# Performance work log

Hardware: AMD Instinct MI355X
Metric: run time of the kernel (lower is better)

Reference implementation:

```python
import jax, jax.numpy as jnp
import numpy as np

D_MODEL = 1024
BATCH = 4
SEQ = 4096

def setup_inputs() -> dict:
    key = jax.random.key(0)
    k1, k2, k3, k4 = jax.random.split(key, 4)
    scale = 1.0 / np.sqrt(D_MODEL)
    return {
        "inp_emb": jax.random.normal(k1, (BATCH, SEQ, D_MODEL), dtype=jnp.float32),
        "Wq": jax.random.normal(k2, (D_MODEL, D_MODEL), dtype=jnp.float32) * scale,
        "Wk": jax.random.normal(k3, (D_MODEL, D_MODEL), dtype=jnp.float32) * scale,
        "Wv": jax.random.normal(k4, (D_MODEL, D_MODEL), dtype=jnp.float32) * scale,
    }

def reference(inp_emb, Wq, Wk, Wv):
    d_model = Wq.shape[0]
    # torch Linear (no bias): y = x @ W.T
    Q = jnp.einsum('bsd,ed->bse', inp_emb, Wq)
    K = jnp.einsum('bsd,ed->bse', inp_emb, Wk)
    V = jnp.einsum('bsd,ed->bse', inp_emb, Wv)
    scores = jnp.einsum('bqd,bkd->bqk', Q, K) / jnp.sqrt(jnp.float32(d_model))
    probs = jax.nn.softmax(scores, axis=2)
    return jnp.einsum('bqk,bkd->bqd', probs, V)
```

## Files before the change

kernel.cpp:

```cpp
#include <hip/hip_runtime.h>


typedef __bf16 bf16_t;
typedef __bf16 bf16x8 __attribute__((ext_vector_type(8)));
typedef float f32x4 __attribute__((ext_vector_type(4)));

typedef __attribute__((address_space(3))) void lds_void_t;
typedef __attribute__((address_space(1))) void gbl_void_t;

#define SEQ 4096
#define DM  1024

__global__ __launch_bounds__(256) void cast_f32_to_bf16(
    const float* __restrict__ in, bf16_t* __restrict__ out, int n8)
{
    int idx = blockIdx.x * 256 + threadIdx.x;
    if (idx >= n8) return;
    long i = (long)idx * 8;
    f32x4 a = *(const f32x4*)(in + i);
    f32x4 b = *(const f32x4*)(in + i + 4);
    bf16x8 o;
    o[0] = (bf16_t)a[0]; o[1] = (bf16_t)a[1]; o[2] = (bf16_t)a[2]; o[3] = (bf16_t)a[3];
    o[4] = (bf16_t)b[0]; o[5] = (bf16_t)b[1]; o[6] = (bf16_t)b[2]; o[7] = (bf16_t)b[3];
    *(bf16x8*)(out + i) = o;
}

__global__ __launch_bounds__(256) void cast3_w(
    const float* __restrict__ w0, const float* __restrict__ w1,
    const float* __restrict__ w2, bf16_t* __restrict__ out)
{
    const float* in = (blockIdx.z == 0) ? w0 : (blockIdx.z == 1) ? w1 : w2;
    long i = ((long)blockIdx.x * 256 + threadIdx.x) * 8;
    f32x4 a = *(const f32x4*)(in + i);
    f32x4 b = *(const f32x4*)(in + i + 4);
    bf16x8 o;
    o[0] = (bf16_t)a[0]; o[1] = (bf16_t)a[1]; o[2] = (bf16_t)a[2]; o[3] = (bf16_t)a[3];
    o[4] = (bf16_t)b[0]; o[5] = (bf16_t)b[1]; o[6] = (bf16_t)b[2]; o[7] = (bf16_t)b[3];
    *(bf16x8*)(out + (long)blockIdx.z * 1048576 + i) = o;
}

__global__ __launch_bounds__(256) void zero_f32(float* __restrict__ p, int n)
{
    int idx = blockIdx.x * 256 + threadIdx.x;
    if (idx < n) p[idx] = 0.f;
}

template <typename TOUT, int MODE>
__global__ __launch_bounds__(256, 4) void gemm_bt(
    const bf16_t* __restrict__ A, int lda, long sAz,
    const bf16_t* __restrict__ B, int ldb, long sBz,
    TOUT* __restrict__ C, int ldc, long sCz,
    int K, float scale, float* __restrict__ l, long sLz)
{
    __shared__ bf16_t As[128 * 32];
    __shared__ bf16_t Bs[128 * 32];

    A += (long)blockIdx.z * sAz;
    B += (long)blockIdx.z * sBz;
    C += (long)blockIdx.z * sCz;

    const int tid  = threadIdx.x;
    const int wave = tid >> 6;
    const int lane = tid & 63;
    const int m0 = blockIdx.x * 128;
    const int n0 = blockIdx.y * 128;
    const int wm = (wave >> 1) * 64;
    const int wn = (wave & 1) * 64;
    const int mrow = lane & 15;
    const int koff = (lane >> 4) * 8;

    f32x4 acc[4][4];
#pragma unroll
    for (int i = 0; i < 4; ++i)
#pragma unroll
        for (int j = 0; j < 4; ++j)
            acc[i][j] = (f32x4){0.f, 0.f, 0.f, 0.f};

    const int c0 = wave * 2;

    for (int k0 = 0; k0 < K; k0 += 32) {
#pragma unroll
        for (int t = 0; t < 2; ++t) {
            const int chunk = c0 + t;
            const int flat  = chunk * 64 + lane;
            const int row   = flat >> 2;
            const int kp    = (flat & 3) * 8;
            const bf16_t* ga = A + (long)(m0 + row) * lda + (k0 + kp);
            const bf16_t* gb = B + (long)(n0 + row) * ldb + (k0 + kp);
            __builtin_amdgcn_global_load_lds((const gbl_void_t*)ga,
                                             (lds_void_t*)(As + chunk * 512), 16, 0, 0);
            __builtin_amdgcn_global_load_lds((const gbl_void_t*)gb,
                                             (lds_void_t*)(Bs + chunk * 512), 16, 0, 0);
        }
        __syncthreads();

        bf16x8 af[4], bfr[4];
#pragma unroll
        for (int i = 0; i < 4; ++i)
            af[i] = *(const bf16x8*)(As + (wm + i * 16 + mrow) * 32 + koff);
#pragma unroll
        for (int j = 0; j < 4; ++j)
            bfr[j] = *(const bf16x8*)(Bs + (wn + j * 16 + mrow) * 32 + koff);
#pragma unroll
        for (int i = 0; i < 4; ++i)
#pragma unroll
            for (int j = 0; j < 4; ++j)
                acc[i][j] = __builtin_amdgcn_mfma_f32_16x16x32_bf16(af[i], bfr[j], acc[i][j], 0, 0, 0);
        __syncthreads();
    }

    const int col = lane & 15;
    const int r0  = (lane >> 4) * 4;

    if (MODE == 1) {
#pragma unroll
        for (int i = 0; i < 4; ++i)
#pragma unroll
            for (int r = 0; r < 4; ++r) {
                float s = 0.f;
#pragma unroll
                for (int j = 0; j < 4; ++j) {
                    float e = __expf(acc[i][j][r] * scale);
                    acc[i][j][r] = e;
                    s += e;
                }
                s += __shfl_xor(s, 1);
                s += __shfl_xor(s, 2);
                s += __shfl_xor(s, 4);
                s += __shfl_xor(s, 8);
                if (col == 0)
                    atomicAdd(&l[(long)blockIdx.z * sLz + m0 + wm + i * 16 + r0 + r], s);
            }
#pragma unroll
        for (int i = 0; i < 4; ++i)
#pragma unroll
            for (int j = 0; j < 4; ++j)
#pragma unroll
                for (int r = 0; r < 4; ++r)
                    C[(long)(m0 + wm + i * 16 + r0 + r) * ldc + (n0 + wn + j * 16 + col)] =
                        (TOUT)acc[i][j][r];
    } else if (MODE == 2) {
        float inv[4][4];
#pragma unroll
        for (int i = 0; i < 4; ++i)
#pragma unroll
            for (int r = 0; r < 4; ++r)
                inv[i][r] = scale / l[(long)blockIdx.z * sLz + m0 + wm + i * 16 + r0 + r];
#pragma unroll
        for (int i = 0; i < 4; ++i)
#pragma unroll
            for (int j = 0; j < 4; ++j)
#pragma unroll
                for (int r = 0; r < 4; ++r)
                    C[(long)(m0 + wm + i * 16 + r0 + r) * ldc + (n0 + wn + j * 16 + col)] =
                        (TOUT)(acc[i][j][r] * inv[i][r]);
    } else {
#pragma unroll
        for (int i = 0; i < 4; ++i)
#pragma unroll
            for (int j = 0; j < 4; ++j)
#pragma unroll
                for (int r = 0; r < 4; ++r)
                    C[(long)(m0 + wm + i * 16 + r0 + r) * ldc + (n0 + wn + j * 16 + col)] =
                        (TOUT)(acc[i][j][r] * scale);
    }
}

template <typename TOUT, int MODE>
__global__ __launch_bounds__(512, 2) void gemm_bt256(
    const bf16_t* __restrict__ A, int lda, long sAz,
    const bf16_t* __restrict__ B, int ldb, long sBz,
    TOUT* __restrict__ C, int ldc, long sCz,
    int K, float scale, float* __restrict__ l, long sLz)
{
    __shared__ __align__(1024) char smem[98304];

    A += (long)blockIdx.z * sAz;
    B += (long)blockIdx.z * sBz;
    C += (long)blockIdx.z * sCz;

    const int tid  = threadIdx.x;
    const int wave = tid >> 6;
    const int lane = tid & 63;
    const int m0 = blockIdx.x * 256;
    const int n0 = blockIdx.y * 256;
    const int wm = (wave >> 2) * 128;
    const int wn = (wave & 3) * 64;

    const int srow = wave * 16 + (lane >> 2);
    const int skk  = ((lane & 3) * 8) ^ ((lane & 32) ? 16 : 0);
    const bf16_t* gA0 = A + (long)(m0 + srow) * lda + skk;
    const bf16_t* gA1 = A + (long)(m0 + srow + 128) * lda + skk;
    const bf16_t* gB0 = B + (long)(n0 + srow) * ldb + skk;
    const bf16_t* gB1 = B + (long)(n0 + srow + 128) * ldb + skk;
    char* ldsA = smem + wave * 1024;
    char* ldsB = smem + 49152 + wave * 1024;

    auto stage_A = [&](int kt, int d) {
        const int k0 = kt << 5;
        __builtin_amdgcn_global_load_lds((const gbl_void_t*)(gA0 + k0),
                                         (lds_void_t*)(ldsA + d * 16384), 16, 0, 0);
        __builtin_amdgcn_global_load_lds((const gbl_void_t*)(gA1 + k0),
                                         (lds_void_t*)(ldsA + d * 16384 + 8192), 16, 0, 0);
    };
    auto stage_B = [&](int kt, int d) {
        const int k0 = kt << 5;
        __builtin_amdgcn_global_load_lds((const gbl_void_t*)(gB0 + k0),
                                         (lds_void_t*)(ldsB + d * 16384), 16, 0, 0);
        __builtin_amdgcn_global_load_lds((const gbl_void_t*)(gB1 + k0),
                                         (lds_void_t*)(ldsB + d * 16384 + 8192), 16, 0, 0);
    };

    const int kswz = ((lane >> 4) * 16) ^ ((lane & 8) ? 32 : 0);
    const int aoff = (wm + (lane & 15)) * 64 + kswz;
    const int boff = (wn + (lane & 15)) * 64 + kswz;

    f32x4 acc[8][4];
#pragma unroll
    for (int i = 0; i < 8; ++i)
#pragma unroll
        for (int j = 0; j < 4; ++j)
            acc[i][j] = (f32x4){0.f, 0.f, 0.f, 0.f};

    const int NT = K >> 5;

    stage_A(0, 0); stage_B(0, 0);
    if (NT > 1) {
        stage_A(1, 1); stage_B(1, 1);
        asm volatile("s_waitcnt vmcnt(4)" ::: "memory");
    } else {
        asm volatile("s_waitcnt vmcnt(0)" ::: "memory");
    }
    __builtin_amdgcn_s_barrier();

    int cur = 0, nxt = 2;
    for (int t = 0; t < NT; ++t) {
        const char* pa = smem + cur * 16384 + aoff;
        const char* pb = smem + 49152 + cur * 16384 + boff;

        bf16x8 bfr[4], af[4];
#pragma unroll
        for (int j = 0; j < 4; ++j) bfr[j] = *(const bf16x8*)(pb + j * 1024);
#pragma unroll
        for (int i = 0; i < 4; ++i) af[i] = *(const bf16x8*)(pa + i * 1024);
        if (t + 2 < NT) stage_A(t + 2, nxt);
        __builtin_amdgcn_s_setprio(1);
#pragma unroll
        for (int i = 0; i < 4; ++i)
#pragma unroll
            for (int j = 0; j < 4; ++j)
                acc[i][j] = __builtin_amdgcn_mfma_f32_16x16x32_bf16(af[i], bfr[j], acc[i][j], 0, 0, 0);
        __builtin_amdgcn_s_setprio(0);

        bf16x8 af2[4];
#pragma unroll
        for (int i = 0; i < 4; ++i) af2[i] = *(const bf16x8*)(pa + 4096 + i * 1024);
        if (t + 2 < NT) stage_B(t + 2, nxt);
        __builtin_amdgcn_s_setprio(1);
#pragma unroll
        for (int i = 0; i < 4; ++i)
#pragma unroll
            for (int j = 0; j < 4; ++j)
                acc[4 + i][j] = __builtin_amdgcn_mfma_f32_16x16x32_bf16(af2[i], bfr[j], acc[4 + i][j], 0, 0, 0);
        __builtin_amdgcn_s_setprio(0);

        __builtin_amdgcn_sched_barrier(0);
        if (t + 2 < NT)
            asm volatile("s_waitcnt vmcnt(4) lgkmcnt(0)" ::: "memory");
        else if (t + 1 < NT)
            asm volatile("s_waitcnt vmcnt(0) lgkmcnt(0)" ::: "memory");
        else
            asm volatile("s_waitcnt lgkmcnt(0)" ::: "memory");
        __builtin_amdgcn_s_barrier();
        cur = (cur == 2) ? 0 : cur + 1;
        nxt = (nxt == 2) ? 0 : nxt + 1;
    }

    const int col = lane & 15;
    const int r0  = (lane >> 4) * 4;

    if (MODE == 1) {
#pragma unroll
        for (int i = 0; i < 8; ++i)
#pragma unroll
            for (int r = 0; r < 4; ++r) {
                float s = 0.f;
#pragma unroll
                for (int j = 0; j < 4; ++j) {
                    float e = __expf(acc[i][j][r] * scale);
                    acc[i][j][r] = e;
                    s += e;
                }
                s += __shfl_xor(s, 1);
                s += __shfl_xor(s, 2);
                s += __shfl_xor(s, 4);
                s += __shfl_xor(s, 8);
                if (col == 0)
                    atomicAdd(&l[(long)blockIdx.z * sLz + m0 + wm + i * 16 + r0 + r], s);
            }
#pragma unroll
        for (int i = 0; i < 8; ++i)
#pragma unroll
            for (int j = 0; j < 4; ++j)
#pragma unroll
                for (int r = 0; r < 4; ++r)
                    C[(long)(m0 + wm + i * 16 + r0 + r) * ldc + (n0 + wn + j * 16 + col)] =
                        (TOUT)acc[i][j][r];
    } else if (MODE == 2) {
        float inv[8][4];
#pragma unroll
        for (int i = 0; i < 8; ++i)
#pragma unroll
            for (int r = 0; r < 4; ++r)
                inv[i][r] = scale / l[(long)blockIdx.z * sLz + m0 + wm + i * 16 + r0 + r];
#pragma unroll
        for (int i = 0; i < 8; ++i)
#pragma unroll
            for (int j = 0; j < 4; ++j)
#pragma unroll
                for (int r = 0; r < 4; ++r)
                    C[(long)(m0 + wm + i * 16 + r0 + r) * ldc + (n0 + wn + j * 16 + col)] =
                        (TOUT)(acc[i][j][r] * inv[i][r]);
    } else {
#pragma unroll
        for (int i = 0; i < 8; ++i)
#pragma unroll
            for (int j = 0; j < 4; ++j)
#pragma unroll
                for (int r = 0; r < 4; ++r)
                    C[(long)(m0 + wm + i * 16 + r0 + r) * ldc + (n0 + wn + j * 16 + col)] =
                        (TOUT)(acc[i][j][r] * scale);
    }
}

__device__ __forceinline__ float waveMax(float v)
{
#pragma unroll
    for (int o = 32; o > 0; o >>= 1) v = fmaxf(v, __shfl_xor(v, o));
    return v;
}
__device__ __forceinline__ float waveSum(float v)
{
#pragma unroll
    for (int o = 32; o > 0; o >>= 1) v += __shfl_xor(v, o);
    return v;
}

__global__ __launch_bounds__(256) void softmax_rows(bf16_t* __restrict__ S)
{
    const long row = blockIdx.x;
    bf16_t* p = S + row * SEQ;
    const int tid = threadIdx.x;

    float v[16];
    bf16x8 a0 = *(const bf16x8*)(p + tid * 16);
    bf16x8 a1 = *(const bf16x8*)(p + tid * 16 + 8);
#pragma unroll
    for (int i = 0; i < 8; ++i) { v[i] = (float)a0[i]; v[8 + i] = (float)a1[i]; }

    float m = -1e30f;
#pragma unroll
    for (int i = 0; i < 16; ++i) m = fmaxf(m, v[i]);

    __shared__ float redm[4];
    __shared__ float reds[4];
    m = waveMax(m);
    if ((tid & 63) == 0) redm[tid >> 6] = m;
    __syncthreads();
    m = fmaxf(fmaxf(redm[0], redm[1]), fmaxf(redm[2], redm[3]));

    float s = 0.f;
#pragma unroll
    for (int i = 0; i < 16; ++i) { v[i] = __expf(v[i] - m); s += v[i]; }
    s = waveSum(s);
    if ((tid & 63) == 0) reds[tid >> 6] = s;
    __syncthreads();
    s = reds[0] + reds[1] + reds[2] + reds[3];
    const float inv = 1.0f / s;

    bf16x8 o0, o1;
#pragma unroll
    for (int i = 0; i < 8; ++i) {
        o0[i] = (bf16_t)(v[i] * inv);
        o1[i] = (bf16_t)(v[8 + i] * inv);
    }
    *(bf16x8*)(p + tid * 16)     = o0;
    *(bf16x8*)(p + tid * 16 + 8) = o1;
}

__global__ __launch_bounds__(256) void transpose_bf16(
    const bf16_t* __restrict__ in, int ldin, long sInZ,
    bf16_t* __restrict__ out, int ldout, long sOutZ)
{
    in  += (long)blockIdx.z * sInZ;
    out += (long)blockIdx.z * sOutZ;
    __shared__ bf16_t t[32][33];
    const int tx = threadIdx.x;
    const int ty = threadIdx.y;
    const int x  = blockIdx.x * 32 + tx;
    const int y0 = blockIdx.y * 32;
#pragma unroll
    for (int i = 0; i < 4; ++i)
        t[ty + i * 8][tx] = in[(long)(y0 + ty + i * 8) * ldin + x];
    __syncthreads();
    const int xo = blockIdx.x * 32;
#pragma unroll
    for (int i = 0; i < 4; ++i)
        out[(long)(xo + ty + i * 8) * ldout + y0 + tx] = t[tx][ty + i * 8];
}

extern "C" void kernel_launch(void* const* d_in, const int* in_sizes, int n_in,
                              void* d_out, int out_size, void* d_ws, size_t ws_size,
                              hipStream_t stream)
{
    const float* X  = (const float*)d_in[0];
    const float* Wq = (const float*)d_in[1];
    const float* Wk = (const float*)d_in[2];
    const float* Wv = (const float*)d_in[3];
    float* out = (float*)d_out;
    char* ws = (char*)d_ws;

    if (ws_size >= (256ull << 20)) {
        bf16_t* Xbf  = (bf16_t*)ws;
        bf16_t* Vbf  = (bf16_t*)(ws + (32l << 20));
        bf16_t* Tbuf = (bf16_t*)(ws + (32l << 20));
        bf16_t* VT   = (bf16_t*)(ws + (64l << 20));
        bf16_t* Sbuf = (bf16_t*)(ws + (96l << 20));
        bf16_t* Wall = (bf16_t*)(ws + (224l << 20));
        bf16_t* WqT  = (bf16_t*)(ws + (230l << 20));
        bf16_t* WkT  = (bf16_t*)(ws + (232l << 20));
        bf16_t* Mt   = (bf16_t*)(ws + (234l << 20));
        float*  lbuf = (float*)(ws + (236l << 20));

        cast_f32_to_bf16<<<(16777216 / 8) / 256, 256, 0, stream>>>(X, Xbf, 16777216 / 8);
        cast3_w<<<dim3(512, 1, 3), 256, 0, stream>>>(Wq, Wk, Wv, Wall);

        transpose_bf16<<<dim3(32, 32, 2), dim3(32, 8), 0, stream>>>(
            Wall, DM, 1048576, WqT, DM, 1048576);

        gemm_bt<bf16_t, 0><<<dim3(8, 8, 1), 256, 0, stream>>>(
            WkT, DM, 0l, WqT, DM, 0l, Mt, DM, 0l, DM, 1.0f, nullptr, 0l);

        gemm_bt256<bf16_t, 0><<<dim3(64, 4, 1), 512, 0, stream>>>(
            Xbf, DM, 0l, Wall + 2097152, DM, 0l, Vbf, DM, 0l, DM, 1.0f, nullptr, 0l);

        transpose_bf16<<<dim3(DM / 32, SEQ / 32, 4), dim3(32, 8), 0, stream>>>(
            Vbf, DM, (long)SEQ * DM, VT, SEQ, (long)DM * SEQ);

        gemm_bt256<bf16_t, 0><<<dim3(64, 4, 1), 512, 0, stream>>>(
            Xbf, DM, 0l, Mt, DM, 0l, Tbuf, DM, 0l, DM, 1.0f, nullptr, 0l);

        zero_f32<<<64, 256, 0, stream>>>(lbuf, 4 * SEQ);

        gemm_bt256<bf16_t, 1><<<dim3(16, 16, 4), 512, 0, stream>>>(
            Tbuf, DM, (long)SEQ * DM,
            Xbf, DM, (long)SEQ * DM,
            Sbuf, SEQ, (long)SEQ * SEQ, DM, 0.03125f, lbuf, SEQ);

        gemm_bt256<float, 2><<<dim3(16, 4, 4), 512, 0, stream>>>(
            Sbuf, SEQ, (long)SEQ * SEQ,
            VT, SEQ, (long)DM * SEQ,
            out, DM, (long)SEQ * DM, SEQ, 1.0f, lbuf, SEQ);
    } else {
        bf16_t* Sbuf = (bf16_t*)ws;
        bf16_t* Xbf  = (bf16_t*)ws;
        bf16_t* Wall = (bf16_t*)(ws + (33l << 20));
        bf16_t* QKV  = (bf16_t*)(ws + (40l << 20));
        bf16_t* VT   = (bf16_t*)(ws + (137l << 20));

        cast_f32_to_bf16<<<(16777216 / 8) / 256, 256, 0, stream>>>(X, Xbf, 16777216 / 8);
        cast3_w<<<dim3(512, 1, 3), 256, 0, stream>>>(Wq, Wk, Wv, Wall);

        gemm_bt<bf16_t, 0><<<dim3(128, 24, 1), 256, 0, stream>>>(
            Xbf, DM, 0l, Wall, DM, 0l, QKV, 3072, 0l, DM, 1.0f, nullptr, 0l);

        for (int b = 0; b < 4; ++b) {
            const bf16_t* Qb = QKV + (long)b * SEQ * 3072;
            gemm_bt<bf16_t, 0><<<dim3(32, 32, 1), 256, 0, stream>>>(
                Qb, 3072, 0l, Qb + 1024, 3072, 0l, Sbuf, SEQ, 0l, DM, 0.03125f, nullptr, 0l);
            softmax_rows<<<SEQ, 256, 0, stream>>>(Sbuf);
            transpose_bf16<<<dim3(DM / 32, SEQ / 32, 1), dim3(32, 8), 0, stream>>>(
                Qb + 2048, 3072, 0l, VT, SEQ, 0l);
            gemm_bt<float, 0><<<dim3(32, 8, 1), 256, 0, stream>>>(
                Sbuf, SEQ, 0l, VT, SEQ, 0l, out + (long)b * SEQ * DM, DM, 0l, SEQ, 1.0f, nullptr, 0l);
        }
    }
}
```

Before: 519.0 us.

## Restructure 256x256 GEMM mainloop to BK=64 double buffering with interleaved staging

```diff
diff --git a/kernel.cpp b/kernel.cpp
--- a/kernel.cpp
+++ b/kernel.cpp
@@ -173,7 +173,7 @@
     TOUT* __restrict__ C, int ldc, long sCz,
     int K, float scale, float* __restrict__ l, long sLz)
 {
-    __shared__ __align__(1024) char smem[98304];
+    __shared__ __align__(1024) char smem[131072];
 
     A += (long)blockIdx.z * sAz;
     B += (long)blockIdx.z * sBz;
@@ -187,33 +187,14 @@
     const int wm = (wave >> 2) * 128;
     const int wn = (wave & 3) * 64;
 
-    const int srow = wave * 16 + (lane >> 2);
-    const int skk  = ((lane & 3) * 8) ^ ((lane & 32) ? 16 : 0);
-    const bf16_t* gA0 = A + (long)(m0 + srow) * lda + skk;
-    const bf16_t* gA1 = A + (long)(m0 + srow + 128) * lda + skk;
-    const bf16_t* gB0 = B + (long)(n0 + srow) * ldb + skk;
-    const bf16_t* gB1 = B + (long)(n0 + srow + 128) * ldb + skk;
-    char* ldsA = smem + wave * 1024;
-    char* ldsB = smem + 49152 + wave * 1024;
-
-    auto stage_A = [&](int kt, int d) {
-        const int k0 = kt << 5;
-        __builtin_amdgcn_global_load_lds((const gbl_void_t*)(gA0 + k0),
-                                         (lds_void_t*)(ldsA + d * 16384), 16, 0, 0);
-        __builtin_amdgcn_global_load_lds((const gbl_void_t*)(gA1 + k0),
-                                         (lds_void_t*)(ldsA + d * 16384 + 8192), 16, 0, 0);
-    };
-    auto stage_B = [&](int kt, int d) {
-        const int k0 = kt << 5;
-        __builtin_amdgcn_global_load_lds((const gbl_void_t*)(gB0 + k0),
-                                         (lds_void_t*)(ldsB + d * 16384), 16, 0, 0);
-        __builtin_amdgcn_global_load_lds((const gbl_void_t*)(gB1 + k0),
-                                         (lds_void_t*)(ldsB + d * 16384 + 8192), 16, 0, 0);
-    };
-
-    const int kswz = ((lane >> 4) * 16) ^ ((lane & 8) ? 32 : 0);
-    const int aoff = (wm + (lane & 15)) * 64 + kswz;
-    const int boff = (wn + (lane & 15)) * 64 + kswz;
+    const int ksw = ((lane & 7) ^ (lane >> 3)) * 8;
+    const bf16_t* gAr = A + (long)(m0 + wave * 8 + (lane >> 3)) * lda + ksw;
+    const bf16_t* gBr = B + (long)(n0 + wave * 8 + (lane >> 3)) * ldb + ksw;
+    const int ldsw = wave * 1024;
+
+    const int kterm = ((lane >> 4) * 16) ^ ((lane & 7) << 4);
+    const int aoff = (wm + (lane & 15)) * 128 + kterm;
+    const int boff = (wn + (lane & 15)) * 128 + kterm;
 
     f32x4 acc[8][4];
 #pragma unroll
@@ -222,59 +203,107 @@
         for (int j = 0; j < 4; ++j)
             acc[i][j] = (f32x4){0.f, 0.f, 0.f, 0.f};
 
-    const int NT = K >> 5;
-
-    stage_A(0, 0); stage_B(0, 0);
-    if (NT > 1) {
-        stage_A(1, 1); stage_B(1, 1);
-        asm volatile("s_waitcnt vmcnt(4)" ::: "memory");
-    } else {
-        asm volatile("s_waitcnt vmcnt(0)" ::: "memory");
+    const int NT = K >> 6;
+
+#define STAGE_A(buf, k0e, s)                                                   \
+    __builtin_amdgcn_global_load_lds(                                          \
+        (const gbl_void_t*)(gAr + (long)(s)*64 * lda + (k0e)),                 \
+        (lds_void_t*)(smem + (buf)*32768 + (s)*8192 + ldsw), 16, 0, 0)
+#define STAGE_B(buf, k0e, s)                                                   \
+    __builtin_amdgcn_global_load_lds(                                          \
+        (const gbl_void_t*)(gBr + (long)(s)*64 * ldb + (k0e)),                 \
+        (lds_void_t*)(smem + 65536 + (buf)*32768 + (s)*8192 + ldsw), 16, 0, 0)
+
+    STAGE_B(0, 0, 0); STAGE_B(0, 0, 1); STAGE_B(0, 0, 2); STAGE_B(0, 0, 3);
+    STAGE_A(0, 0, 0); STAGE_A(0, 0, 2); STAGE_A(0, 0, 1); STAGE_A(0, 0, 3);
+    asm volatile("s_waitcnt vmcnt(2)" ::: "memory");
+    __builtin_amdgcn_sched_barrier(0);
+    __builtin_amdgcn_s_barrier();
+
+    for (int t = 0; t < NT; ++t) {
+        const int cb = t & 1;
+        const int nb = cb ^ 1;
+        const char* Ac = smem + cb * 32768;
+        const char* Bc = smem + 65536 + cb * 32768;
+        const bool more = (t + 1 < NT);
+        const int kn = (t + 1) << 6;
+
+        bf16x8 b0[4], b1[4], af[4];
+
+#pragma unroll
+        for (int j = 0; j < 4; ++j) b0[j] = *(const bf16x8*)(Bc + boff + j * 2048);
+#pragma unroll
+        for (int i = 0; i < 4; ++i) af[i] = *(const bf16x8*)(Ac + aoff + i * 2048);
+        if (more) { STAGE_B(nb, kn, 0); STAGE_B(nb, kn, 1); }
+        __builtin_amdgcn_s_barrier();
+        asm volatile("s_waitcnt lgkmcnt(0)" ::: "memory");
+        __builtin_amdgcn_sched_barrier(0);
+        __builtin_amdgcn_s_setprio(1);
+#pragma unroll
+        for (int i = 0; i < 4; ++i)
+#pragma unroll
+            for (int j = 0; j < 4; ++j)
+                acc[i][j] = __builtin_amdgcn_mfma_f32_16x16x32_bf16(af[i], b0[j], acc[i][j], 0, 0, 0);
+        __builtin_amdgcn_s_setprio(0);
+        __builtin_amdgcn_s_barrier();
+
+#pragma unroll
+        for (int j = 0; j < 4; ++j) b1[j] = *(const bf16x8*)(Bc + (boff ^ 64) + j * 2048);
+#pragma unroll
+        for (int i = 0; i < 4; ++i) af[i] = *(const bf16x8*)(Ac + (aoff ^ 64) + i * 2048);
+        if (more) { STAGE_B(nb, kn, 2); STAGE_B(nb, kn, 3); }
+        __builtin_amdgcn_s_barrier();
+        asm volatile("s_waitcnt lgkmcnt(0)" ::: "memory");
+        __builtin_amdgcn_sched_barrier(0);
+        __builtin_amdgcn_s_setprio(1);
+#pragma unroll
+        for (int i = 0; i < 4; ++i)
+#pragma unroll
+            for (int j = 0; j < 4; ++j)
+                acc[i][j] = __builtin_amdgcn_mfma_f32_16x16x32_bf16(af[i], b1[j], acc[i][j], 0, 0, 0);
+        __builtin_amdgcn_s_setprio(0);
+        if (more)
+            asm volatile("s_waitcnt vmcnt(4)" ::: "memory");
+        else
+            asm volatile("s_waitcnt vmcnt(0)" ::: "memory");
+        __builtin_amdgcn_sched_barrier(0);
+        __builtin_amdgcn_s_barrier();
+
+#pragma unroll
+        for (int i = 0; i < 4; ++i) af[i] = *(const bf16x8*)(Ac + aoff + 8192 + i * 2048);
+        if (more) { STAGE_A(nb, kn, 0); STAGE_A(nb, kn, 2); }
+        __builtin_amdgcn_s_barrier();
+        asm volatile("s_waitcnt lgkmcnt(0)" ::: "memory");
+        __builtin_amdgcn_sched_barrier(0);
+        __builtin_amdgcn_s_setprio(1);
+#pragma unroll
+        for (int i = 0; i < 4; ++i)
+#pragma unroll
+            for (int j = 0; j < 4; ++j)
+                acc[4 + i][j] = __builtin_amdgcn_mfma_f32_16x16x32_bf16(af[i], b0[j], acc[4 + i][j], 0, 0, 0);
+        __builtin_amdgcn_s_setprio(0);
+        __builtin_amdgcn_s_barrier();
+
+#pragma unroll
+        for (int i = 0; i < 4; ++i) af[i] = *(const bf16x8*)(Ac + (aoff ^ 64) + 8192 + i * 2048);
+        if (more) { STAGE_A(nb, kn, 1); STAGE_A(nb, kn, 3); }
+        __builtin_amdgcn_s_barrier();
+        asm volatile("s_waitcnt lgkmcnt(0)" ::: "memory");
+        __builtin_amdgcn_sched_barrier(0);
+        __builtin_amdgcn_s_setprio(1);
+#pragma unroll
+        for (int i = 0; i < 4; ++i)
+#pragma unroll
+            for (int j = 0; j < 4; ++j)
+                acc[4 + i][j] = __builtin_amdgcn_mfma_f32_16x16x32_bf16(af[i], b1[j], acc[4 + i][j], 0, 0, 0);
+        __builtin_amdgcn_s_setprio(0);
+        if (more)
+            asm volatile("s_waitcnt vmcnt(2)" ::: "memory");
+        __builtin_amdgcn_sched_barrier(0);
+        __builtin_amdgcn_s_barrier();
     }
-    __builtin_amdgcn_s_barrier();
-
-    int cur = 0, nxt = 2;
-    for (int t = 0; t < NT; ++t) {
-        const char* pa = smem + cur * 16384 + aoff;
-        const char* pb = smem + 49152 + cur * 16384 + boff;
-
-        bf16x8 bfr[4], af[4];
-#pragma unroll
-        for (int j = 0; j < 4; ++j) bfr[j] = *(const bf16x8*)(pb + j * 1024);
-#pragma unroll
-        for (int i = 0; i < 4; ++i) af[i] = *(const bf16x8*)(pa + i * 1024);
-        if (t + 2 < NT) stage_A(t + 2, nxt);
-        __builtin_amdgcn_s_setprio(1);
-#pragma unroll
-        for (int i = 0; i < 4; ++i)
-#pragma unroll
-            for (int j = 0; j < 4; ++j)
-                acc[i][j] = __builtin_amdgcn_mfma_f32_16x16x32_bf16(af[i], bfr[j], acc[i][j], 0, 0, 0);
-        __builtin_amdgcn_s_setprio(0);
-
-        bf16x8 af2[4];
-#pragma unroll
-        for (int i = 0; i < 4; ++i) af2[i] = *(const bf16x8*)(pa + 4096 + i * 1024);
-        if (t + 2 < NT) stage_B(t + 2, nxt);
-        __builtin_amdgcn_s_setprio(1);
-#pragma unroll
-        for (int i = 0; i < 4; ++i)
-#pragma unroll
-            for (int j = 0; j < 4; ++j)
-                acc[4 + i][j] = __builtin_amdgcn_mfma_f32_16x16x32_bf16(af2[i], bfr[j], acc[4 + i][j], 0, 0, 0);
-        __builtin_amdgcn_s_setprio(0);
-
-        __builtin_amdgcn_sched_barrier(0);
-        if (t + 2 < NT)
-            asm volatile("s_waitcnt vmcnt(4) lgkmcnt(0)" ::: "memory");
-        else if (t + 1 < NT)
-            asm volatile("s_waitcnt vmcnt(0) lgkmcnt(0)" ::: "memory");
-        else
-            asm volatile("s_waitcnt lgkmcnt(0)" ::: "memory");
-        __builtin_amdgcn_s_barrier();
-        cur = (cur == 2) ? 0 : cur + 1;
-        nxt = (nxt == 2) ? 0 : nxt + 1;
-    }
+#undef STAGE_A
+#undef STAGE_B
 
     const int col = lane & 15;
     const int r0  = (lane >> 4) * 4;
```

Measured after the change: 524.5 us. Within noise of the previous version (+1.1%).

## Shrink GEMM tile to 256x128 for higher occupancy with new LDS swizzle

Applied to the files above, without the earlier changes.

```diff
diff --git a/kernel.cpp b/kernel.cpp
--- a/kernel.cpp
+++ b/kernel.cpp
@@ -166,14 +166,14 @@
     }
 }
 
-template <typename TOUT, int MODE>
-__global__ __launch_bounds__(512, 2) void gemm_bt256(
-    const bf16_t* __restrict__ A, int lda, long sAz,
-    const bf16_t* __restrict__ B, int ldb, long sBz,
-    TOUT* __restrict__ C, int ldc, long sCz,
+template <typename TOUT, int MODE, int LDA, int LDB, int LDC>
+__global__ __launch_bounds__(512, 4) void gemm_bt256(
+    const bf16_t* __restrict__ A, long sAz,
+    const bf16_t* __restrict__ B, long sBz,
+    TOUT* __restrict__ C, long sCz,
     int K, float scale, float* __restrict__ l, long sLz)
 {
-    __shared__ __align__(1024) char smem[98304];
+    __shared__ __align__(1024) char smem[73728];
 
     A += (long)blockIdx.z * sAz;
     B += (long)blockIdx.z * sBz;
@@ -183,98 +183,99 @@
     const int wave = tid >> 6;
     const int lane = tid & 63;
     const int m0 = blockIdx.x * 256;
-    const int n0 = blockIdx.y * 256;
+    const int n0 = blockIdx.y * 128;
     const int wm = (wave >> 2) * 128;
-    const int wn = (wave & 3) * 64;
+    const int wn = (wave & 3) * 32;
 
     const int srow = wave * 16 + (lane >> 2);
-    const int skk  = ((lane & 3) * 8) ^ ((lane & 32) ? 16 : 0);
-    const bf16_t* gA0 = A + (long)(m0 + srow) * lda + skk;
-    const bf16_t* gA1 = A + (long)(m0 + srow + 128) * lda + skk;
-    const bf16_t* gB0 = B + (long)(n0 + srow) * ldb + skk;
-    const bf16_t* gB1 = B + (long)(n0 + srow + 128) * ldb + skk;
-    char* ldsA = smem + wave * 1024;
-    char* ldsB = smem + 49152 + wave * 1024;
-
-    auto stage_A = [&](int kt, int d) {
-        const int k0 = kt << 5;
-        __builtin_amdgcn_global_load_lds((const gbl_void_t*)(gA0 + k0),
-                                         (lds_void_t*)(ldsA + d * 16384), 16, 0, 0);
-        __builtin_amdgcn_global_load_lds((const gbl_void_t*)(gA1 + k0),
-                                         (lds_void_t*)(ldsA + d * 16384 + 8192), 16, 0, 0);
-    };
-    auto stage_B = [&](int kt, int d) {
-        const int k0 = kt << 5;
-        __builtin_amdgcn_global_load_lds((const gbl_void_t*)(gB0 + k0),
-                                         (lds_void_t*)(ldsB + d * 16384), 16, 0, 0);
-        __builtin_amdgcn_global_load_lds((const gbl_void_t*)(gB1 + k0),
-                                         (lds_void_t*)(ldsB + d * 16384 + 8192), 16, 0, 0);
-    };
-
-    const int kswz = ((lane >> 4) * 16) ^ ((lane & 8) ? 32 : 0);
-    const int aoff = (wm + (lane & 15)) * 64 + kswz;
-    const int boff = (wn + (lane & 15)) * 64 + kswz;
-
-    f32x4 acc[8][4];
+    const int ksrc = (((lane & 3) ^ ((lane >> 3) & 3)) << 3);
+    const bf16_t* pa0 = A + (long)(m0 + srow) * LDA + ksrc;
+    const bf16_t* pa1 = pa0 + (long)128 * LDA;
+    const bf16_t* pb0 = B + (long)(n0 + srow) * LDB + ksrc;
+    const int ldsw = wave * 1024;
+
+    const int kterm = (((lane >> 4) ^ ((lane >> 1) & 3)) << 4);
+    const int aoff = (wm + (lane & 15)) * 64 + kterm;
+    const int boff = (wn + (lane & 15)) * 64 + kterm;
+
+    f32x4 acc[8][2];
 #pragma unroll
     for (int i = 0; i < 8; ++i)
 #pragma unroll
-        for (int j = 0; j < 4; ++j)
+        for (int j = 0; j < 2; ++j)
             acc[i][j] = (f32x4){0.f, 0.f, 0.f, 0.f};
 
     const int NT = K >> 5;
 
-    stage_A(0, 0); stage_B(0, 0);
+#define STAGE_A2(buf)                                                          \
+    do {                                                                       \
+        __builtin_amdgcn_global_load_lds((const gbl_void_t*)pa0,               \
+            (lds_void_t*)(smem + (buf)*16384 + ldsw), 16, 0, 0);               \
+        __builtin_amdgcn_global_load_lds((const gbl_void_t*)pa1,               \
+            (lds_void_t*)(smem + (buf)*16384 + 8192 + ldsw), 16, 0, 0);        \
+    } while (0)
+#define STAGE_B1(buf)                                                          \
+    __builtin_amdgcn_global_load_lds((const gbl_void_t*)pb0,                   \
+        (lds_void_t*)(smem + 49152 + (buf)*8192 + ldsw), 16, 0, 0)
+
+    STAGE_A2(0); STAGE_B1(0); pa0 += 32; pa1 += 32; pb0 += 32;
     if (NT > 1) {
-        stage_A(1, 1); stage_B(1, 1);
-        asm volatile("s_waitcnt vmcnt(4)" ::: "memory");
+        STAGE_A2(1); STAGE_B1(1); pa0 += 32; pa1 += 32; pb0 += 32;
+        asm volatile("s_waitcnt vmcnt(3)" ::: "memory");
     } else {
         asm volatile("s_waitcnt vmcnt(0)" ::: "memory");
     }
+    __builtin_amdgcn_sched_barrier(0);
     __builtin_amdgcn_s_barrier();
 
-    int cur = 0, nxt = 2;
+    int cur = 0, sb = 2;
     for (int t = 0; t < NT; ++t) {
-        const char* pa = smem + cur * 16384 + aoff;
-        const char* pb = smem + 49152 + cur * 16384 + boff;
-
-        bf16x8 bfr[4], af[4];
-#pragma unroll
-        for (int j = 0; j < 4; ++j) bfr[j] = *(const bf16x8*)(pb + j * 1024);
-#pragma unroll
-        for (int i = 0; i < 4; ++i) af[i] = *(const bf16x8*)(pa + i * 1024);
-        if (t + 2 < NT) stage_A(t + 2, nxt);
+        const char* Ab = smem + cur * 16384;
+        const char* Bb = smem + 49152 + cur * 8192;
+        const bool more = (t + 2 < NT);
+
+        bf16x8 bfr[2], af[4];
+#pragma unroll
+        for (int j = 0; j < 2; ++j) bfr[j] = *(const bf16x8*)(Bb + boff + j * 1024);
+#pragma unroll
+        for (int i = 0; i < 4; ++i) af[i] = *(const bf16x8*)(Ab + aoff + i * 1024);
+        if (more) STAGE_A2(sb);
+        asm volatile("s_waitcnt lgkmcnt(0)" ::: "memory");
+        __builtin_amdgcn_sched_barrier(0);
         __builtin_amdgcn_s_setprio(1);
 #pragma unroll
         for (int i = 0; i < 4; ++i)
 #pragma unroll
-            for (int j = 0; j < 4; ++j)
+            for (int j = 0; j < 2; ++j)
                 acc[i][j] = __builtin_amdgcn_mfma_f32_16x16x32_bf16(af[i], bfr[j], acc[i][j], 0, 0, 0);
         __builtin_amdgcn_s_setprio(0);
 
-        bf16x8 af2[4];
-#pragma unroll
-        for (int i = 0; i < 4; ++i) af2[i] = *(const bf16x8*)(pa + 4096 + i * 1024);
-        if (t + 2 < NT) stage_B(t + 2, nxt);
+#pragma unroll
+        for (int i = 0; i < 4; ++i) af[i] = *(const bf16x8*)(Ab + aoff + 4096 + i * 1024);
+        if (more) STAGE_B1(sb);
+        asm volatile("s_waitcnt lgkmcnt(0)" ::: "memory");
+        __builtin_amdgcn_sched_barrier(0);
         __builtin_amdgcn_s_setprio(1);
 #pragma unroll
         for (int i = 0; i < 4; ++i)
 #pragma unroll
-            for (int j = 0; j < 4; ++j)
-                acc[4 + i][j] = __builtin_amdgcn_mfma_f32_16x16x32_bf16(af2[i], bfr[j], acc[4 + i][j], 0, 0, 0);
+            for (int j = 0; j < 2; ++j)
+                acc[4 + i][j] = __builtin_amdgcn_mfma_f32_16x16x32_bf16(af[i], bfr[j], acc[4 + i][j], 0, 0, 0);
         __builtin_amdgcn_s_setprio(0);
 
+        if (more) {
+            asm volatile("s_waitcnt vmcnt(3)" ::: "memory");
+            pa0 += 32; pa1 += 32; pb0 += 32;
+        } else if (t + 1 < NT) {
+            asm volatile("s_waitcnt vmcnt(0)" ::: "memory");
+        }
         __builtin_amdgcn_sched_barrier(0);
-        if (t + 2 < NT)
-            asm volatile("s_waitcnt vmcnt(4) lgkmcnt(0)" ::: "memory");
-        else if (t + 1 < NT)
-            asm volatile("s_waitcnt vmcnt(0) lgkmcnt(0)" ::: "memory");
-        else
-            asm volatile("s_waitcnt lgkmcnt(0)" ::: "memory");
         __builtin_amdgcn_s_barrier();
         cur = (cur == 2) ? 0 : cur + 1;
-        nxt = (nxt == 2) ? 0 : nxt + 1;
-    }
+        sb  = (sb == 2) ? 0 : sb + 1;
+    }
+#undef STAGE_A2
+#undef STAGE_B1
 
     const int col = lane & 15;
     const int r0  = (lane >> 4) * 4;
@@ -286,7 +287,7 @@
             for (int r = 0; r < 4; ++r) {
                 float s = 0.f;
 #pragma unroll
-                for (int j = 0; j < 4; ++j) {
+                for (int j = 0; j < 2; ++j) {
                     float e = __expf(acc[i][j][r] * scale);
                     acc[i][j][r] = e;
                     s += e;
@@ -301,10 +302,10 @@
 #pragma unroll
         for (int i = 0; i < 8; ++i)
 #pragma unroll
-            for (int j = 0; j < 4; ++j)
-#pragma unroll
-                for (int r = 0; r < 4; ++r)
-                    C[(long)(m0 + wm + i * 16 + r0 + r) * ldc + (n0 + wn + j * 16 + col)] =
+            for (int j = 0; j < 2; ++j)
+#pragma unroll
+                for (int r = 0; r < 4; ++r)
+                    C[(long)(m0 + wm + i * 16 + r0 + r) * LDC + (n0 + wn + j * 16 + col)] =
                         (TOUT)acc[i][j][r];
     } else if (MODE == 2) {
         float inv[8][4];
@@ -316,19 +317,19 @@
 #pragma unroll
         for (int i = 0; i < 8; ++i)
 #pragma unroll
-            for (int j = 0; j < 4; ++j)
-#pragma unroll
-                for (int r = 0; r < 4; ++r)
-                    C[(long)(m0 + wm + i * 16 + r0 + r) * ldc + (n0 + wn + j * 16 + col)] =
+            for (int j = 0; j < 2; ++j)
+#pragma unroll
+                for (int r = 0; r < 4; ++r)
+                    C[(long)(m0 + wm + i * 16 + r0 + r) * LDC + (n0 + wn + j * 16 + col)] =
                         (TOUT)(acc[i][j][r] * inv[i][r]);
     } else {
 #pragma unroll
         for (int i = 0; i < 8; ++i)
 #pragma unroll
-            for (int j = 0; j < 4; ++j)
-#pragma unroll
-                for (int r = 0; r < 4; ++r)
-                    C[(long)(m0 + wm + i * 16 + r0 + r) * ldc + (n0 + wn + j * 16 + col)] =
+            for (int j = 0; j < 2; ++j)
+#pragma unroll
+                for (int r = 0; r < 4; ++r)
+                    C[(long)(m0 + wm + i * 16 + r0 + r) * LDC + (n0 + wn + j * 16 + col)] =
                         (TOUT)(acc[i][j][r] * scale);
     }
 }
@@ -441,26 +442,26 @@
         gemm_bt<bf16_t, 0><<<dim3(8, 8, 1), 256, 0, stream>>>(
             WkT, DM, 0l, WqT, DM, 0l, Mt, DM, 0l, DM, 1.0f, nullptr, 0l);
 
-        gemm_bt256<bf16_t, 0><<<dim3(64, 4, 1), 512, 0, stream>>>(
-            Xbf, DM, 0l, Wall + 2097152, DM, 0l, Vbf, DM, 0l, DM, 1.0f, nullptr, 0l);
+        gemm_bt256<bf16_t, 0, DM, DM, DM><<<dim3(64, 8, 1), 512, 0, stream>>>(
+            Xbf, 0l, Wall + 2097152, 0l, Vbf, 0l, DM, 1.0f, nullptr, 0l);
 
         transpose_bf16<<<dim3(DM / 32, SEQ / 32, 4), dim3(32, 8), 0, stream>>>(
             Vbf, DM, (long)SEQ * DM, VT, SEQ, (long)DM * SEQ);
 
-        gemm_bt256<bf16_t, 0><<<dim3(64, 4, 1), 512, 0, stream>>>(
-            Xbf, DM, 0l, Mt, DM, 0l, Tbuf, DM, 0l, DM, 1.0f, nullptr, 0l);
+        gemm_bt256<bf16_t, 0, DM, DM, DM><<<dim3(64, 8, 1), 512, 0, stream>>>(
+            Xbf, 0l, Mt, 0l, Tbuf, 0l, DM, 1.0f, nullptr, 0l);
 
         zero_f32<<<64, 256, 0, stream>>>(lbuf, 4 * SEQ);
 
-        gemm_bt256<bf16_t, 1><<<dim3(16, 16, 4), 512, 0, stream>>>(
-            Tbuf, DM, (long)SEQ * DM,
-            Xbf, DM, (long)SEQ * DM,
-            Sbuf, SEQ, (long)SEQ * SEQ, DM, 0.03125f, lbuf, SEQ);
-
-        gemm_bt256<float, 2><<<dim3(16, 4, 4), 512, 0, stream>>>(
-            Sbuf, SEQ, (long)SEQ * SEQ,
-            VT, SEQ, (long)DM * SEQ,
-            out, DM, (long)SEQ * DM, SEQ, 1.0f, lbuf, SEQ);
+        gemm_bt256<bf16_t, 1, DM, DM, SEQ><<<dim3(16, 32, 4), 512, 0, stream>>>(
+            Tbuf, (long)SEQ * DM,
+            Xbf, (long)SEQ * DM,
+            Sbuf, (long)SEQ * SEQ, DM, 0.03125f, lbuf, SEQ);
+
+        gemm_bt256<float, 2, SEQ, SEQ, DM><<<dim3(16, 8, 4), 512, 0, stream>>>(
+            Sbuf, (long)SEQ * SEQ,
+            VT, (long)DM * SEQ,
+            out, (long)SEQ * DM, SEQ, 1.0f, lbuf, SEQ);
     } else {
         bf16_t* Sbuf = (bf16_t*)ws;
         bf16_t* Xbf  = (bf16_t*)ws;
```

Result: slower. 545.7 us (+5.1%).
